# Kernel optimization log

Measured on AMD Instinct MI355X. Metric: run time of the kernel, lower is better.

## Reference

```python
import jax, jax.numpy as jnp
import numpy as np

EPS = 1e-8
N_GENRES = 10


def gelu(x):
    return jax.nn.gelu(x, approximate=False)  # torch nn.GELU default = exact erf


def setup_inputs() -> dict:
    B, IN_DIM, DIM = 4096, 512, 1024
    key = jax.random.key(0)
    ks = jax.random.split(key, 14)
    inp = {
        "noise": jax.random.normal(ks[0], (B, IN_DIM), dtype=jnp.float32),  # unused (dead arg in original)
        "genre_batch": jax.random.randint(ks[1], (B,), 0, N_GENRES),
        "z": jax.random.normal(ks[2], (B, IN_DIM), dtype=jnp.float32),  # reparam noise for torch.normal
        # per-genre distribution params
        "mu_table": jax.random.normal(ks[3], (N_GENRES, IN_DIM), dtype=jnp.float32),
        "sigma_table": jax.random.normal(ks[4], (N_GENRES, IN_DIM), dtype=jnp.float32),
        # shared MLP: in_dim -> dim -> dim
        "Ws1": jax.random.normal(ks[5], (IN_DIM, DIM), dtype=jnp.float32) * (1.0 / np.sqrt(IN_DIM)),
        "bs1": jnp.zeros((DIM,), dtype=jnp.float32),
        "Ws2": jax.random.normal(ks[6], (DIM, DIM), dtype=jnp.float32) * (1.0 / np.sqrt(DIM)),
        "bs2": jnp.zeros((DIM,), dtype=jnp.float32),
        # 10 unshared expert MLPs: dim -> dim -> dim
        "We1": jax.random.normal(ks[7], (N_GENRES, DIM, DIM), dtype=jnp.float32) * (1.0 / np.sqrt(DIM)),
        "be1": jnp.zeros((N_GENRES, DIM), dtype=jnp.float32),
        "We2": jax.random.normal(ks[8], (N_GENRES, DIM, DIM), dtype=jnp.float32) * (1.0 / np.sqrt(DIM)),
        "be2": jnp.zeros((N_GENRES, DIM), dtype=jnp.float32),
    }
    return inp


def reference(noise, genre_batch, z, mu_table, sigma_table,
              Ws1, bs1, Ws2, bs2, We1, be1, We2, be2):
    # per-sample gather of genre mu/sigma, then reparameterized normal sample
    mu = mu_table[genre_batch]                              # [B, in_dim]
    std = jnp.abs(sigma_table[genre_batch]) + EPS           # [B, in_dim]
    noise_genre = mu + std * z                              # ~ Normal(mu, std)

    # shared MLP
    s = gelu(noise_genre @ Ws1 + bs1)                       # [B, dim]
    s = gelu(s @ Ws2 + bs2)                                 # [B, dim]

    # per-sample expert dispatch: compute all 10 experts densely, select by genre
    h = gelu(jnp.einsum('bd,edh->ebh', s, We1) + be1[:, None, :])   # [E, B, dim]
    o = jnp.einsum('ebh,eho->ebo', h, We2) + be2[:, None, :]        # [E, B, dim]
    out = o[genre_batch, jnp.arange(s.shape[0])]            # [B, dim]
    return out
```

## Files before the change

### kernel.cpp

```cpp
#include <hip/hip_runtime.h>
#include <hip/hip_bf16.h>

typedef __bf16 bf16;
typedef __bf16 bf16x8 __attribute__((ext_vector_type(8)));
typedef float floatx4 __attribute__((ext_vector_type(4)));

#define B_ROWS 4096
#define IN_DIM 512
#define DIM 1024
#define NG 10

__device__ __forceinline__ float geluf(float x) {
    return 0.5f * x * (1.0f + erff(x * 0.70710678118654752f));
}

__device__ __forceinline__ void async16(void* lds, const void* g) {
    __builtin_amdgcn_global_load_lds(
        (const __attribute__((address_space(1))) unsigned int*)g,
        (__attribute__((address_space(3))) unsigned int*)lds, 16, 0, 0);
}

__global__ void prep_kernel(const int* __restrict__ genre,
                            const float* __restrict__ z,
                            const float* __restrict__ mu_t,
                            const float* __restrict__ sg_t,
                            bf16* __restrict__ ng) {
    const int t = blockIdx.x * 256 + threadIdx.x;
    const int row = t >> 6;
    const int c0 = (t & 63) * 8;
    const int g = genre[row];
    const float* zp = z + (size_t)row * IN_DIM + c0;
    const float* mp = mu_t + (size_t)g * IN_DIM + c0;
    const float* sp = sg_t + (size_t)g * IN_DIM + c0;
    floatx4 z0 = *(const floatx4*)zp, z1 = *(const floatx4*)(zp + 4);
    floatx4 m0 = *(const floatx4*)mp, m1 = *(const floatx4*)(mp + 4);
    floatx4 s0 = *(const floatx4*)sp, s1 = *(const floatx4*)(sp + 4);
    bf16x8 o;
#pragma unroll
    for (int i = 0; i < 4; i++) {
        o[i] = (bf16)(m0[i] + (fabsf(s0[i]) + 1e-8f) * z0[i]);
        o[i + 4] = (bf16)(m1[i] + (fabsf(s1[i]) + 1e-8f) * z1[i]);
    }
    *(bf16x8*)(ng + (size_t)row * IN_DIM + c0) = o;
}

__global__ void bucket_kernel(const int* __restrict__ genre,
                              int* __restrict__ counts,
                              int* __restrict__ offsets,
                              int* __restrict__ row_ids) {
    __shared__ int hist[NG];
    __shared__ int base[NG];
    const int tid = threadIdx.x;
    if (tid < NG) hist[tid] = 0;
    __syncthreads();
    int g[4];
#pragma unroll
    for (int i = 0; i < 4; i++) {
        g[i] = genre[tid + i * 1024];
        atomicAdd(&hist[g[i]], 1);
    }
    __syncthreads();
    if (tid == 0) {
        int acc = 0;
        for (int e = 0; e < NG; e++) {
            base[e] = acc;
            counts[e] = hist[e];
            offsets[e] = acc;
            acc += hist[e];
        }
        offsets[NG] = acc;
    }
    __syncthreads();
    if (tid < NG) hist[tid] = base[tid];
    __syncthreads();
#pragma unroll
    for (int i = 0; i < 4; i++) {
        int pos = atomicAdd(&hist[g[i]], 1);
        row_ids[pos] = tid + i * 1024;
    }
}

__global__ void transpose_all_kernel(const float* __restrict__ Ws1,
                                     const float* __restrict__ Ws2,
                                     const float* __restrict__ We1,
                                     const float* __restrict__ We2,
                                     bf16* __restrict__ WT1,
                                     bf16* __restrict__ WT2,
                                     bf16* __restrict__ WE1T,
                                     bf16* __restrict__ WE2T) {
    int b = blockIdx.x;
    const float* src;
    bf16* dst;
    int R;
    if (b < 512) {
        src = Ws1; dst = WT1; R = 512;
    } else if (b < 1536) {
        b -= 512; src = Ws2; dst = WT2; R = 1024;
    } else if (b < 11776) {
        b -= 1536;
        int e = b >> 10; b &= 1023;
        src = We1 + (size_t)e * DIM * DIM;
        dst = WE1T + (size_t)e * DIM * DIM;
        R = 1024;
    } else {
        b -= 11776;
        int e = b >> 10; b &= 1023;
        src = We2 + (size_t)e * DIM * DIM;
        dst = WE2T + (size_t)e * DIM * DIM;
        R = 1024;
    }
    const int c0 = (b & 31) * 32;
    const int r0 = (b >> 5) * 32;
    __shared__ float t[32][33];
#pragma unroll
    for (int i = threadIdx.y; i < 32; i += 8)
        t[i][threadIdx.x] = src[(size_t)(r0 + i) * 1024 + c0 + threadIdx.x];
    __syncthreads();
#pragma unroll
    for (int i = threadIdx.y; i < 32; i += 8)
        dst[(size_t)(c0 + i) * R + r0 + threadIdx.x] = (bf16)t[threadIdx.x][i];
}

template <bool EXPERT, bool GATHER_A, bool SCATTER_C, bool GELU, typename CT>
__global__ __launch_bounds__(256, 4) void gemm_kernel(
    const bf16* __restrict__ A, const bf16* __restrict__ BT,
    const float* __restrict__ bias, CT* __restrict__ Cmat,
    int M, int N, int K,
    const int* __restrict__ row_ids, const int* __restrict__ offsets,
    const int* __restrict__ counts) {
    int off = 0, cnt = M;
    if (EXPERT) {
        const int g = blockIdx.z;
        cnt = counts[g];
        if ((int)blockIdx.y * 64 >= cnt) return;
        off = offsets[g];
        BT += (size_t)g * N * K;
        bias += (size_t)g * N;
    }
    const int m_start = blockIdx.y * 64;
    const int n0 = blockIdx.x * 64;

    constexpr int BK = 128;
    __shared__ bf16 As[64 * BK];
    __shared__ bf16 Bs[64 * BK];

    const int tid = threadIdx.x;
    const int lane = tid & 63;
    const int wave = tid >> 6;
    const int wrow = (wave >> 1) * 32;
    const int wcol = (wave & 1) * 32;
    const int quad = lane >> 4;
    const int l16 = lane & 15;

    const bf16* a_src[4];
    const bf16* b_src[4];
    bf16* a_dst[4];
    bf16* b_dst[4];
#pragma unroll
    for (int i = 0; i < 4; i++) {
        const int s = i * 256 + tid;
        const int row = s >> 4;
        const int col = ((s & 15) ^ (row & 15)) * 8;
        const int sbase = i * 256 + wave * 64;
        a_dst[i] = As + sbase * 8;
        b_dst[i] = Bs + sbase * 8;
        int p = m_start + row;
        size_t arow;
        if (EXPERT) {
            int pp = off + min(p, cnt - 1);
            arow = GATHER_A ? (size_t)row_ids[pp] : (size_t)pp;
        } else {
            arow = (size_t)p;
        }
        a_src[i] = A + arow * (size_t)K + col;
        b_src[i] = BT + (size_t)(n0 + row) * K + col;
    }

    floatx4 acc[2][2];
#pragma unroll
    for (int i = 0; i < 2; i++)
#pragma unroll
        for (int j = 0; j < 2; j++)
#pragma unroll
            for (int r = 0; r < 4; r++) acc[i][j][r] = 0.0f;

    const int nK = K / BK;
    for (int kt = 0; kt < nK; kt++) {
        const int kbase = kt * BK;
#pragma unroll
        for (int i = 0; i < 4; i++) async16(a_dst[i], a_src[i] + kbase);
#pragma unroll
        for (int i = 0; i < 4; i++) async16(b_dst[i], b_src[i] + kbase);
        __syncthreads();
#pragma unroll
        for (int ks = 0; ks < 4; ks++) {
            bf16x8 af[2], bfr[2];
            const int cb = ks * 4 + quad;
#pragma unroll
            for (int i = 0; i < 2; i++) {
                const int r = wrow + i * 16 + l16;
                af[i] = *(const bf16x8*)(As + (r * 16 + (cb ^ (r & 15))) * 8);
            }
#pragma unroll
            for (int j = 0; j < 2; j++) {
                const int n = wcol + j * 16 + l16;
                bfr[j] = *(const bf16x8*)(Bs + (n * 16 + (cb ^ (n & 15))) * 8);
            }
#pragma unroll
            for (int i = 0; i < 2; i++)
#pragma unroll
                for (int j = 0; j < 2; j++)
                    acc[i][j] = __builtin_amdgcn_mfma_f32_16x16x32_bf16(
                        af[i], bfr[j], acc[i][j], 0, 0, 0);
        }
        __syncthreads();
    }

#pragma unroll
    for (int j = 0; j < 2; j++) {
        const int n = n0 + wcol + j * 16 + l16;
        const float bv = bias[n];
#pragma unroll
        for (int i = 0; i < 2; i++) {
            const int rbase = wrow + i * 16 + quad * 4;
#pragma unroll
            for (int r = 0; r < 4; r++) {
                const int p = m_start + rbase + r;
                if (EXPERT && p >= cnt) continue;
                float v = acc[i][j][r] + bv;
                if (GELU) v = geluf(v);
                size_t drow;
                if (EXPERT) {
                    const int pp = off + p;
                    drow = SCATTER_C ? (size_t)row_ids[pp] : (size_t)pp;
                } else {
                    drow = (size_t)p;
                }
                Cmat[drow * (size_t)N + n] = (CT)v;
            }
        }
    }
}

extern "C" void kernel_launch(void* const* d_in, const int* in_sizes, int n_in,
                              void* d_out, int out_size, void* d_ws,
                              size_t ws_size, hipStream_t stream) {
    const int* genre = (const int*)d_in[1];
    const float* z = (const float*)d_in[2];
    const float* mu_t = (const float*)d_in[3];
    const float* sg_t = (const float*)d_in[4];
    const float* Ws1 = (const float*)d_in[5];
    const float* bs1 = (const float*)d_in[6];
    const float* Ws2 = (const float*)d_in[7];
    const float* bs2 = (const float*)d_in[8];
    const float* We1 = (const float*)d_in[9];
    const float* be1 = (const float*)d_in[10];
    const float* We2 = (const float*)d_in[11];
    const float* be2 = (const float*)d_in[12];
    float* out = (float*)d_out;

    char* w = (char*)d_ws;
    int* counts = (int*)w;
    int* offsets = (int*)(w + 256);
    int* row_ids = (int*)(w + 1024);
    char* wb = w + (64 << 10);
    bf16* ng = (bf16*)wb;
    bf16* hp = (bf16*)wb;
    bf16* s1 = (bf16*)(wb + ((size_t)4 << 20));
    bf16* s2 = (bf16*)(wb + ((size_t)12 << 20));
    bf16* WT1 = (bf16*)(wb + ((size_t)20 << 20));
    bf16* WT2 = WT1 + (size_t)IN_DIM * DIM;
    bf16* WE1T = WT2 + (size_t)DIM * DIM;
    bf16* WE2T = WE1T + (size_t)NG * DIM * DIM;

    bucket_kernel<<<1, 1024, 0, stream>>>(genre, counts, offsets, row_ids);
    prep_kernel<<<B_ROWS * IN_DIM / 8 / 256, 256, 0, stream>>>(genre, z, mu_t,
                                                               sg_t, ng);
    transpose_all_kernel<<<22016, dim3(32, 8), 0, stream>>>(
        Ws1, Ws2, We1, We2, WT1, WT2, WE1T, WE2T);

    gemm_kernel<false, false, false, true, bf16>
        <<<dim3(DIM / 64, B_ROWS / 64), 256, 0, stream>>>(
            ng, WT1, bs1, s1, B_ROWS, DIM, IN_DIM, nullptr, nullptr, nullptr);
    gemm_kernel<false, false, false, true, bf16>
        <<<dim3(DIM / 64, B_ROWS / 64), 256, 0, stream>>>(
            s1, WT2, bs2, s2, B_ROWS, DIM, DIM, nullptr, nullptr, nullptr);
    gemm_kernel<true, true, false, true, bf16>
        <<<dim3(DIM / 64, B_ROWS / 64, NG), 256, 0, stream>>>(
            s2, WE1T, be1, hp, B_ROWS, DIM, DIM, row_ids, offsets, counts);
    gemm_kernel<true, false, true, false, float>
        <<<dim3(DIM / 64, B_ROWS / 64, NG), 256, 0, stream>>>(
            hp, WE2T, be2, out, B_ROWS, DIM, DIM, row_ids, offsets, counts);
}
```

Before: 262.4 us.

## Enlarge GEMM tile to 128x64 and vectorize weight transpose with 64x64 tiles

The GEMM block tile grows from 64x64 to 128x64, so each wave computes a 64x32 sub-tile with 4x2 MFMA accumulators. This raises arithmetic intensity per LDS load and halves the number of blocks, and the bigger LDS and register use may lower occupancy. The weight transpose/convert kernel now handles 64x64 tiles with float4 loads, an XOR-swizzled LDS layout, and 16-byte bf16 stores, which should cut memory transactions in what is likely a large share of the runtime. Expert groups with few rows waste more of the larger M tile.

```diff
diff --git a/kernel.cpp b/kernel.cpp
--- a/kernel.cpp
+++ b/kernel.cpp
@@ -91,34 +91,50 @@
     int b = blockIdx.x;
     const float* src;
     bf16* dst;
-    int R;
-    if (b < 512) {
-        src = Ws1; dst = WT1; R = 512;
-    } else if (b < 1536) {
-        b -= 512; src = Ws2; dst = WT2; R = 1024;
-    } else if (b < 11776) {
-        b -= 1536;
-        int e = b >> 10; b &= 1023;
+    int R, ty;
+    if (b < 128) {
+        src = Ws1; dst = WT1; R = 512; ty = b >> 4; b &= 15;
+    } else if (b < 384) {
+        b -= 128; src = Ws2; dst = WT2; R = 1024; ty = b >> 4; b &= 15;
+    } else if (b < 2944) {
+        b -= 384;
+        int e = b >> 8; b &= 255;
         src = We1 + (size_t)e * DIM * DIM;
         dst = WE1T + (size_t)e * DIM * DIM;
-        R = 1024;
+        R = 1024; ty = b >> 4; b &= 15;
     } else {
-        b -= 11776;
-        int e = b >> 10; b &= 1023;
+        b -= 2944;
+        int e = b >> 8; b &= 255;
         src = We2 + (size_t)e * DIM * DIM;
         dst = WE2T + (size_t)e * DIM * DIM;
-        R = 1024;
-    }
-    const int c0 = (b & 31) * 32;
-    const int r0 = (b >> 5) * 32;
-    __shared__ float t[32][33];
-#pragma unroll
-    for (int i = threadIdx.y; i < 32; i += 8)
-        t[i][threadIdx.x] = src[(size_t)(r0 + i) * 1024 + c0 + threadIdx.x];
-    __syncthreads();
-#pragma unroll
-    for (int i = threadIdx.y; i < 32; i += 8)
-        dst[(size_t)(c0 + i) * R + r0 + threadIdx.x] = (bf16)t[threadIdx.x][i];
+        R = 1024; ty = b >> 4; b &= 15;
+    }
+    const int r0 = ty * 64, c0 = b * 64;
+    __shared__ float T[64 * 64];
+    const int tid = threadIdx.x;
+#pragma unroll
+    for (int i = 0; i < 4; i++) {
+        const int s = i * 256 + tid;
+        const int r = s >> 4;
+        const int cv = s & 15;
+        floatx4 v = *(const floatx4*)(src + (size_t)(r0 + r) * 1024 + c0 + cv * 4);
+        *(floatx4*)(T + r * 64 + ((cv ^ (r >> 3)) * 4)) = v;
+    }
+    __syncthreads();
+#pragma unroll
+    for (int i = 0; i < 2; i++) {
+        const int s = i * 256 + tid;
+        const int oc = s >> 3;
+        const int og = s & 7;
+        const int cg = oc >> 2, o = oc & 3;
+        bf16x8 v;
+#pragma unroll
+        for (int t = 0; t < 8; t++) {
+            const int r = og * 8 + t;
+            v[t] = (bf16)T[r * 64 + ((cg ^ (r >> 3)) * 4) + o];
+        }
+        *(bf16x8*)(dst + (size_t)(c0 + oc) * R + r0 + og * 8) = v;
+    }
 }
 
 template <bool EXPERT, bool GATHER_A, bool SCATTER_C, bool GELU, typename CT>
@@ -132,38 +148,34 @@
     if (EXPERT) {
         const int g = blockIdx.z;
         cnt = counts[g];
-        if ((int)blockIdx.y * 64 >= cnt) return;
+        if ((int)blockIdx.y * 128 >= cnt) return;
         off = offsets[g];
         BT += (size_t)g * N * K;
         bias += (size_t)g * N;
     }
-    const int m_start = blockIdx.y * 64;
+    const int m_start = blockIdx.y * 128;
     const int n0 = blockIdx.x * 64;
 
     constexpr int BK = 128;
-    __shared__ bf16 As[64 * BK];
+    __shared__ bf16 As[128 * BK];
     __shared__ bf16 Bs[64 * BK];
 
     const int tid = threadIdx.x;
     const int lane = tid & 63;
     const int wave = tid >> 6;
-    const int wrow = (wave >> 1) * 32;
+    const int wrow = (wave >> 1) * 64;
     const int wcol = (wave & 1) * 32;
     const int quad = lane >> 4;
     const int l16 = lane & 15;
 
-    const bf16* a_src[4];
-    const bf16* b_src[4];
-    bf16* a_dst[4];
-    bf16* b_dst[4];
-#pragma unroll
-    for (int i = 0; i < 4; i++) {
+    const bf16* a_src[8];
+    bf16* a_dst[8];
+#pragma unroll
+    for (int i = 0; i < 8; i++) {
         const int s = i * 256 + tid;
         const int row = s >> 4;
         const int col = ((s & 15) ^ (row & 15)) * 8;
-        const int sbase = i * 256 + wave * 64;
-        a_dst[i] = As + sbase * 8;
-        b_dst[i] = Bs + sbase * 8;
+        a_dst[i] = As + (i * 256 + wave * 64) * 8;
         int p = m_start + row;
         size_t arow;
         if (EXPERT) {
@@ -173,12 +185,21 @@
             arow = (size_t)p;
         }
         a_src[i] = A + arow * (size_t)K + col;
+    }
+    const bf16* b_src[4];
+    bf16* b_dst[4];
+#pragma unroll
+    for (int i = 0; i < 4; i++) {
+        const int s = i * 256 + tid;
+        const int row = s >> 4;
+        const int col = ((s & 15) ^ (row & 15)) * 8;
+        b_dst[i] = Bs + (i * 256 + wave * 64) * 8;
         b_src[i] = BT + (size_t)(n0 + row) * K + col;
     }
 
-    floatx4 acc[2][2];
-#pragma unroll
-    for (int i = 0; i < 2; i++)
+    floatx4 acc[4][2];
+#pragma unroll
+    for (int i = 0; i < 4; i++)
 #pragma unroll
         for (int j = 0; j < 2; j++)
 #pragma unroll
@@ -188,16 +209,16 @@
     for (int kt = 0; kt < nK; kt++) {
         const int kbase = kt * BK;
 #pragma unroll
-        for (int i = 0; i < 4; i++) async16(a_dst[i], a_src[i] + kbase);
+        for (int i = 0; i < 8; i++) async16(a_dst[i], a_src[i] + kbase);
 #pragma unroll
         for (int i = 0; i < 4; i++) async16(b_dst[i], b_src[i] + kbase);
         __syncthreads();
 #pragma unroll
         for (int ks = 0; ks < 4; ks++) {
-            bf16x8 af[2], bfr[2];
+            bf16x8 af[4], bfr[2];
             const int cb = ks * 4 + quad;
 #pragma unroll
-            for (int i = 0; i < 2; i++) {
+            for (int i = 0; i < 4; i++) {
                 const int r = wrow + i * 16 + l16;
                 af[i] = *(const bf16x8*)(As + (r * 16 + (cb ^ (r & 15))) * 8);
             }
@@ -207,7 +228,7 @@
                 bfr[j] = *(const bf16x8*)(Bs + (n * 16 + (cb ^ (n & 15))) * 8);
             }
 #pragma unroll
-            for (int i = 0; i < 2; i++)
+            for (int i = 0; i < 4; i++)
 #pragma unroll
                 for (int j = 0; j < 2; j++)
                     acc[i][j] = __builtin_amdgcn_mfma_f32_16x16x32_bf16(
@@ -221,7 +242,7 @@
         const int n = n0 + wcol + j * 16 + l16;
         const float bv = bias[n];
 #pragma unroll
-        for (int i = 0; i < 2; i++) {
+        for (int i = 0; i < 4; i++) {
             const int rbase = wrow + i * 16 + quad * 4;
 #pragma unroll
             for (int r = 0; r < 4; r++) {
@@ -276,19 +297,19 @@
     bucket_kernel<<<1, 1024, 0, stream>>>(genre, counts, offsets, row_ids);
     prep_kernel<<<B_ROWS * IN_DIM / 8 / 256, 256, 0, stream>>>(genre, z, mu_t,
                                                                sg_t, ng);
-    transpose_all_kernel<<<22016, dim3(32, 8), 0, stream>>>(
-        Ws1, Ws2, We1, We2, WT1, WT2, WE1T, WE2T);
+    transpose_all_kernel<<<5504, 256, 0, stream>>>(Ws1, Ws2, We1, We2, WT1,
+                                                   WT2, WE1T, WE2T);
 
     gemm_kernel<false, false, false, true, bf16>
-        <<<dim3(DIM / 64, B_ROWS / 64), 256, 0, stream>>>(
+        <<<dim3(DIM / 64, B_ROWS / 128), 256, 0, stream>>>(
             ng, WT1, bs1, s1, B_ROWS, DIM, IN_DIM, nullptr, nullptr, nullptr);
     gemm_kernel<false, false, false, true, bf16>
-        <<<dim3(DIM / 64, B_ROWS / 64), 256, 0, stream>>>(
+        <<<dim3(DIM / 64, B_ROWS / 128), 256, 0, stream>>>(
             s1, WT2, bs2, s2, B_ROWS, DIM, DIM, nullptr, nullptr, nullptr);
     gemm_kernel<true, true, false, true, bf16>
-        <<<dim3(DIM / 64, B_ROWS / 64, NG), 256, 0, stream>>>(
+        <<<dim3(DIM / 64, B_ROWS / 128, NG), 256, 0, stream>>>(
             s2, WE1T, be1, hp, B_ROWS, DIM, DIM, row_ids, offsets, counts);
     gemm_kernel<true, false, true, false, float>
-        <<<dim3(DIM / 64, B_ROWS / 64, NG), 256, 0, stream>>>(
+        <<<dim3(DIM / 64, B_ROWS / 128, NG), 256, 0, stream>>>(
             hp, WE2T, be2, out, B_ROWS, DIM, DIM, row_ids, offsets, counts);
 }
```

New measurement: 254.1 us. -3.2%, faster.
